# Kernel optimization log

Measured on AMD Instinct MI355X. Metric: run time of the kernel, lower is better.

## Reference

```python
import jax, jax.numpy as jnp
import numpy as np

EPS = 1e-8

def dice(x, alpha):
    # Dice activation (dim=3): per-channel BN (batch stats over B,L axes), then gating.
    m = jnp.mean(x, axis=(0, 1), keepdims=True)
    v = jnp.var(x, axis=(0, 1), keepdims=True)
    p = jax.nn.sigmoid((x - m) * jax.lax.rsqrt(v + EPS))
    return p * x + (1.0 - p) * alpha * x


def setup_inputs() -> dict:
    key = jax.random.key(0)
    ks = jax.random.split(key, 12)
    B, L, D = 2048, 200, 128
    H1, H2 = 128, 32
    query = jax.random.normal(ks[0], (B, D), dtype=jnp.float32)
    keys = jax.random.normal(ks[1], (B, L, D), dtype=jnp.float32)
    keys_len = jax.random.randint(ks[2], (B,), 0, L)
    s1 = 1.0 / np.sqrt(4 * D)
    s2 = 1.0 / np.sqrt(H1)
    s3 = 1.0 / np.sqrt(H2)
    W1 = jax.random.uniform(ks[3], (4 * D, H1), minval=-s1, maxval=s1, dtype=jnp.float32)
    b1 = jax.random.uniform(ks[4], (H1,), minval=-s1, maxval=s1, dtype=jnp.float32)
    alpha1 = jnp.zeros((H1,), dtype=jnp.float32)
    W2 = jax.random.uniform(ks[5], (H1, H2), minval=-s2, maxval=s2, dtype=jnp.float32)
    b2 = jax.random.uniform(ks[6], (H2,), minval=-s2, maxval=s2, dtype=jnp.float32)
    alpha2 = jnp.zeros((H2,), dtype=jnp.float32)
    Wd = jax.random.uniform(ks[7], (H2, 1), minval=-s3, maxval=s3, dtype=jnp.float32)
    bd = jax.random.uniform(ks[8], (1,), minval=-s3, maxval=s3, dtype=jnp.float32)
    return {"query": query, "keys": keys, "keys_len": keys_len,
            "W1": W1, "b1": b1, "alpha1": alpha1,
            "W2": W2, "b2": b2, "alpha2": alpha2,
            "Wd": Wd, "bd": bd}


def reference(query, keys, keys_len, W1, b1, alpha1, W2, b2, alpha2, Wd, bd):
    B, L, D = keys.shape
    q = jnp.broadcast_to(query[:, None, :], (B, L, D))
    # concat/diff/product features -> (B, L, 4D)
    x = jnp.concatenate([q, keys, q - keys, q * keys], axis=-1)
    h = dice(x @ W1 + b1, alpha1)
    h = dice(h @ W2 + b2, alpha2)
    score = (h @ Wd + bd)[..., 0]            # (B, L)
    mask = jnp.arange(L) < keys_len[:, None]  # (B, L)
    score = jnp.where(mask, score, 0.0)
    # weighted-sum pooling: (B, L) x (B, L, D) -> (B, D)
    return jnp.einsum('bl,bld->bd', score, keys)
```

## Files before the change

### kernel.cpp

```cpp
#include <hip/hip_runtime.h>
#include <hip/hip_bf16.h>
#include <stdint.h>

typedef __attribute__((ext_vector_type(8))) short bf16x8;
typedef __attribute__((ext_vector_type(4))) float f32x4;

#define B_SZ 2048
#define L_SZ 200
#define D_SZ 128
#define NROWS (B_SZ * L_SZ)
#define NTILES (NROWS / 16)

__device__ __forceinline__ short f2bf(float f) {
    __bf16 h = (__bf16)f;
    return __builtin_bit_cast(short, h);
}
__device__ __forceinline__ float bf2f(short s) {
    union { uint32_t u; float f; } v; v.u = ((uint32_t)(uint16_t)s) << 16;
    return v.f;
}
__device__ __forceinline__ float sigm(float x) {
    return 1.0f / (1.0f + __expf(-x));
}

__global__ void k0_prep(const float* __restrict__ W1, const float* __restrict__ W2,
                        float* __restrict__ Aprime, float* __restrict__ Bf32,
                        float* __restrict__ Cf32, ushort* __restrict__ W2f,
                        float* __restrict__ stats)
{
    const int total = 16384 + 16384 + 16384 + 4096 + 512;
    for (int i = blockIdx.x * blockDim.x + threadIdx.x; i < total; i += gridDim.x * blockDim.x) {
        if (i < 16384) {
            int r = i >> 7, c = i & 127;
            Aprime[i] = W1[r * 128 + c] + W1[(256 + r) * 128 + c];
        } else if (i < 32768) {
            int e = i - 16384;
            int j = e & 7, l = (e >> 3) & 63, kt = (e >> 9) & 3, ct = e >> 11;
            int k = kt * 32 + ((l >> 4) << 3) + j;
            int col = (ct << 4) + (l & 15);
            Bf32[e] = W1[(128 + k) * 128 + col] - W1[(256 + k) * 128 + col];
        } else if (i < 49152) {
            int e = i - 32768;
            int j = e & 7, l = (e >> 3) & 63, kt = (e >> 9) & 3, ct = e >> 11;
            int k = kt * 32 + ((l >> 4) << 3) + j;
            int col = (ct << 4) + (l & 15);
            Cf32[e] = W1[(384 + k) * 128 + col];
        } else if (i < 49152 + 4096) {
            int f = i - 49152;
            int j = f & 7, l = (f >> 3) & 63, kt = (f >> 9) & 3, ct = f >> 11;
            int kk = kt * 32 + ((l >> 4) << 3) + j;
            int col = (ct << 4) + (l & 15);
            W2f[f] = (ushort)f2bf(W2[kk * 32 + col]);
        } else {
            stats[i - (49152 + 4096)] = 0.0f;
        }
    }
}

__global__ void k1_qA(const float* __restrict__ q, const float* __restrict__ Aprime,
                      const float* __restrict__ b1, float* __restrict__ qA)
{
    __shared__ float qs[128];
    int b = blockIdx.x, c = threadIdx.x;
    qs[c] = q[b * 128 + c];
    __syncthreads();
    float acc = b1[c];
    #pragma unroll 8
    for (int r = 0; r < 128; ++r) acc += qs[r] * Aprime[r * 128 + c];
    qA[b * 128 + c] = acc;
}

__global__ void __launch_bounds__(64, 2) k2_main(
    const float* __restrict__ query, const float* __restrict__ keys,
    const float* __restrict__ qA, const float* __restrict__ Bf32,
    const float* __restrict__ Cf32, ushort* __restrict__ z1,
    float* __restrict__ stats1)
{
    const int lane = threadIdx.x;
    const int b = blockIdx.x;
    const int r15 = lane & 15, g = lane >> 4;

    f32x4 qv[4][2];
    #pragma unroll
    for (int kt = 0; kt < 4; ++kt) {
        const float* qp = query + (size_t)b * 128 + kt * 32 + g * 8;
        qv[kt][0] = *(const f32x4*)(qp);
        qv[kt][1] = *(const f32x4*)(qp + 4);
    }

    bf16x8 wb[8][4];
    #pragma unroll
    for (int ct = 0; ct < 8; ++ct)
        #pragma unroll
        for (int kt = 0; kt < 4; ++kt) {
            const int fi = ((ct * 4 + kt) * 64 + lane) * 8;
            f32x4 b0 = *(const f32x4*)(Bf32 + fi);
            f32x4 b1v = *(const f32x4*)(Bf32 + fi + 4);
            f32x4 c0 = *(const f32x4*)(Cf32 + fi);
            f32x4 c1 = *(const f32x4*)(Cf32 + fi + 4);
            bf16x8 w;
            #pragma unroll
            for (int j = 0; j < 4; ++j) {
                w[j]     = f2bf(b0[j]  + qv[kt][0][j] * c0[j]);
                w[4 + j] = f2bf(b1v[j] + qv[kt][1][j] * c1[j]);
            }
            wb[ct][kt] = w;
        }

    float qa[8];
    #pragma unroll
    for (int ct = 0; ct < 8; ++ct) qa[ct] = qA[(size_t)b * 128 + ct * 16 + r15];

    float ssum[8] = {0,0,0,0,0,0,0,0}, ssq[8] = {0,0,0,0,0,0,0,0};

    const float* kbase = keys + (size_t)b * L_SZ * 128;
    ushort* zbase = z1 + (size_t)b * L_SZ * 128;

    for (int t = 0; t < 13; ++t) {
        const int row0 = t * 16;
        const int lrowc = min(row0 + r15, L_SZ - 1);
        const float* kp = kbase + (size_t)lrowc * 128 + g * 8;

        bf16x8 afr[4];
        #pragma unroll
        for (int kt = 0; kt < 4; ++kt) {
            f32x4 k0 = *(const f32x4*)(kp + kt * 32);
            f32x4 k1 = *(const f32x4*)(kp + kt * 32 + 4);
            bf16x8 a;
            #pragma unroll
            for (int j = 0; j < 4; ++j) { a[j] = f2bf(k0[j]); a[4 + j] = f2bf(k1[j]); }
            afr[kt] = a;
        }

        f32x4 acc[8];
        #pragma unroll
        for (int ct = 0; ct < 8; ++ct) {
            acc[ct] = (f32x4){0, 0, 0, 0};
            #pragma unroll
            for (int kt = 0; kt < 4; ++kt)
                acc[ct] = __builtin_amdgcn_mfma_f32_16x16x32_bf16(afr[kt], wb[ct][kt], acc[ct], 0, 0, 0);
        }

        const int rbase = row0 + g * 4;
        #pragma unroll
        for (int j = 0; j < 4; ++j) {
            const int row = rbase + j;
            if (row < L_SZ) {
                #pragma unroll
                for (int ct = 0; ct < 8; ++ct) {
                    float v = acc[ct][j] + qa[ct];
                    ssum[ct] += v;
                    ssq[ct] += v * v;
                    zbase[(size_t)row * 128 + ct * 16 + r15] = (ushort)f2bf(v);
                }
            }
        }
    }

    #pragma unroll
    for (int ct = 0; ct < 8; ++ct) {
        float s = ssum[ct], q2 = ssq[ct];
        s += __shfl_xor(s, 16); s += __shfl_xor(s, 32);
        q2 += __shfl_xor(q2, 16); q2 += __shfl_xor(q2, 32);
        if (g == 0) {
            atomicAdd(&stats1[ct * 16 + r15], s);
            atomicAdd(&stats1[128 + ct * 16 + r15], q2);
        }
    }
}

__global__ void k_fin(const float* __restrict__ raw, float* __restrict__ fin, int nch)
{
    int c = threadIdx.x;
    if (c >= nch) return;
    float n = (float)NROWS;
    float m = raw[c] / n;
    float v = raw[nch + c] / n - m * m;
    float r = rsqrtf(v + 1e-8f);
    fin[c] = r;
    fin[nch + c] = -m * r;
}

__global__ void __launch_bounds__(64, 2) k4_z2(
    const ushort* __restrict__ z1, const ushort* __restrict__ W2f,
    const float* __restrict__ fin1, const float* __restrict__ alpha1,
    const float* __restrict__ b2, float* __restrict__ z2, float* __restrict__ stats2)
{
    const int lane = threadIdx.x, r15 = lane & 15, g = lane >> 4;
    bf16x8 bfr[2][4];
    #pragma unroll
    for (int ct = 0; ct < 2; ++ct)
        #pragma unroll
        for (int kt = 0; kt < 4; ++kt)
            bfr[ct][kt] = *(const bf16x8*)(W2f + ((size_t)(ct * 4 + kt) * 64 + lane) * 8);

    float rstd[4][8], bias0[4][8], alp[4][8];
    #pragma unroll
    for (int kt = 0; kt < 4; ++kt)
        #pragma unroll
        for (int j = 0; j < 8; ++j) {
            int c = kt * 32 + g * 8 + j;
            rstd[kt][j] = fin1[c];
            bias0[kt][j] = fin1[128 + c];
            alp[kt][j] = alpha1[c];
        }
    float b2v[2] = { b2[r15], b2[16 + r15] };
    float ssum[2] = {0, 0}, ssq[2] = {0, 0};

    for (int rt = blockIdx.x; rt < NTILES; rt += gridDim.x) {
        int rowA = rt * 16 + r15;
        bf16x8 afr[4];
        #pragma unroll
        for (int kt = 0; kt < 4; ++kt) {
            bf16x8 zv = *(const bf16x8*)(z1 + (size_t)rowA * 128 + kt * 32 + g * 8);
            bf16x8 hv;
            #pragma unroll
            for (int j = 0; j < 8; ++j) {
                float z = bf2f(zv[j]);
                float zh = z * rstd[kt][j] + bias0[kt][j];
                float p = sigm(zh);
                float t = p + (1.0f - p) * alp[kt][j];
                hv[j] = f2bf(z * t);
            }
            afr[kt] = hv;
        }
        f32x4 acc[2];
        #pragma unroll
        for (int ct = 0; ct < 2; ++ct) {
            acc[ct] = (f32x4){0, 0, 0, 0};
            #pragma unroll
            for (int kt = 0; kt < 4; ++kt)
                acc[ct] = __builtin_amdgcn_mfma_f32_16x16x32_bf16(afr[kt], bfr[ct][kt], acc[ct], 0, 0, 0);
        }
        int rowC = rt * 16 + g * 4;
        #pragma unroll
        for (int j = 0; j < 4; ++j) {
            int row = rowC + j;
            #pragma unroll
            for (int ct = 0; ct < 2; ++ct) {
                float v = acc[ct][j] + b2v[ct];
                ssum[ct] += v;
                ssq[ct] += v * v;
                z2[(size_t)row * 32 + ct * 16 + r15] = v;
            }
        }
    }
    #pragma unroll
    for (int ct = 0; ct < 2; ++ct) {
        float s = ssum[ct], q2 = ssq[ct];
        s += __shfl_xor(s, 16); s += __shfl_xor(s, 32);
        q2 += __shfl_xor(q2, 16); q2 += __shfl_xor(q2, 32);
        if (g == 0) {
            int col = ct * 16 + r15;
            atomicAdd(&stats2[col], s);
            atomicAdd(&stats2[32 + col], q2);
        }
    }
}

__global__ void __launch_bounds__(256) k6_score_pool(
    const float* __restrict__ z2, const float* __restrict__ keys,
    const int* __restrict__ keys_len, const float* __restrict__ fin2,
    const float* __restrict__ alpha2, const float* __restrict__ Wd,
    const float* __restrict__ bd, float* __restrict__ out)
{
    __shared__ float pp[129];
    __shared__ float sc[200];
    __shared__ float part[2][128];
    int b = blockIdx.x, t = threadIdx.x;
    if (t < 64) pp[t] = fin2[t];
    else if (t < 96) pp[t] = alpha2[t - 64];
    else if (t < 128) pp[t] = Wd[t - 96];
    else if (t == 128) pp[128] = bd[0];
    __syncthreads();

    int klen = keys_len[b];
    if (t < 200) {
        float s = 0.0f;
        if (t < klen) {
            const float* zp = z2 + ((size_t)b * 200 + t) * 32;
            f32x4 zr[8];
            #pragma unroll
            for (int i = 0; i < 8; ++i) zr[i] = ((const f32x4*)zp)[i];
            s = pp[128];
            #pragma unroll
            for (int c = 0; c < 32; ++c) {
                float z = zr[c >> 2][c & 3];
                float zh = z * pp[c] + pp[32 + c];
                float p = sigm(zh);
                float h = z * (p + (1.0f - p) * pp[64 + c]);
                s += h * pp[96 + c];
            }
        }
        sc[t] = s;
    }
    __syncthreads();

    int c = t & 127, prt = t >> 7;
    int lim = min(100, klen - prt * 100);
    const float* kp = keys + ((size_t)b * 200 + prt * 100) * 128 + c;
    float acc = 0.0f;
    #pragma unroll 4
    for (int l = 0; l < lim; ++l) acc += sc[prt * 100 + l] * kp[(size_t)l * 128];
    part[prt][c] = acc;
    __syncthreads();
    if (t < 128) out[(size_t)b * 128 + t] = part[0][t] + part[1][t];
}

extern "C" void kernel_launch(void* const* d_in, const int* in_sizes, int n_in,
                              void* d_out, int out_size, void* d_ws, size_t ws_size,
                              hipStream_t stream) {
    const float* query    = (const float*)d_in[0];
    const float* keys     = (const float*)d_in[1];
    const int*   keys_len = (const int*)d_in[2];
    const float* W1       = (const float*)d_in[3];
    const float* b1       = (const float*)d_in[4];
    const float* alpha1   = (const float*)d_in[5];
    const float* W2       = (const float*)d_in[6];
    const float* b2       = (const float*)d_in[7];
    const float* alpha2   = (const float*)d_in[8];
    const float* Wd       = (const float*)d_in[9];
    const float* bd       = (const float*)d_in[10];
    float* out = (float*)d_out;

    char* ws = (char*)d_ws;
    ushort* z1     = (ushort*)(ws);
    float*  z2     = (float*)(ws + 104857600);
    float*  qA     = (float*)(ws + 157286400);
    float*  Aprime = (float*)(ws + 158334976);
    float*  Bf32   = (float*)(ws + 158400512);
    float*  Cf32   = (float*)(ws + 158466048);
    ushort* W2f    = (ushort*)(ws + 158531584);
    float*  stats  = (float*)(ws + 158539776);
    float*  fin1   = (float*)(ws + 158541824);
    float*  fin2   = (float*)(ws + 158542848);

    k0_prep<<<128, 256, 0, stream>>>(W1, W2, Aprime, Bf32, Cf32, W2f, stats);
    k1_qA<<<B_SZ, 128, 0, stream>>>(query, Aprime, b1, qA);
    k2_main<<<B_SZ, 64, 0, stream>>>(query, keys, qA, Bf32, Cf32, z1, stats);
    k_fin<<<1, 128, 0, stream>>>(stats, fin1, 128);
    k4_z2<<<4096, 64, 0, stream>>>(z1, W2f, fin1, alpha1, b2, z2, stats + 256);
    k_fin<<<1, 32, 0, stream>>>(stats + 256, fin2, 32);
    k6_score_pool<<<B_SZ, 256, 0, stream>>>(z2, keys, keys_len, fin2, alpha2, Wd, bd, out);
}
```

Measured before the change: 282.5 us.

## Split k2 across column groups, store z2 as bf16, vectorize k4 param loads

```diff
diff --git a/kernel.cpp b/kernel.cpp
--- a/kernel.cpp
+++ b/kernel.cpp
@@ -3,6 +3,7 @@
 #include <stdint.h>
 
 typedef __attribute__((ext_vector_type(8))) short bf16x8;
+typedef __attribute__((ext_vector_type(8))) unsigned short u16x8;
 typedef __attribute__((ext_vector_type(4))) float f32x4;
 
 #define B_SZ 2048
@@ -70,14 +71,16 @@
     qA[b * 128 + c] = acc;
 }
 
-__global__ void __launch_bounds__(64, 2) k2_main(
+__global__ void __launch_bounds__(64, 4) k2_main(
     const float* __restrict__ query, const float* __restrict__ keys,
     const float* __restrict__ qA, const float* __restrict__ Bf32,
     const float* __restrict__ Cf32, ushort* __restrict__ z1,
     float* __restrict__ stats1)
 {
+    const int p = blockIdx.x;
+    const int b = (p & 7) | ((p >> 5) << 3);
+    const int cg = (p >> 3) & 3;
     const int lane = threadIdx.x;
-    const int b = blockIdx.x;
     const int r15 = lane & 15, g = lane >> 4;
 
     f32x4 qv[4][2];
@@ -88,11 +91,12 @@
         qv[kt][1] = *(const f32x4*)(qp + 4);
     }
 
-    bf16x8 wb[8][4];
-    #pragma unroll
-    for (int ct = 0; ct < 8; ++ct)
+    bf16x8 wb[2][4];
+    #pragma unroll
+    for (int ctl = 0; ctl < 2; ++ctl)
         #pragma unroll
         for (int kt = 0; kt < 4; ++kt) {
+            const int ct = cg * 2 + ctl;
             const int fi = ((ct * 4 + kt) * 64 + lane) * 8;
             f32x4 b0 = *(const f32x4*)(Bf32 + fi);
             f32x4 b1v = *(const f32x4*)(Bf32 + fi + 4);
@@ -104,14 +108,15 @@
                 w[j]     = f2bf(b0[j]  + qv[kt][0][j] * c0[j]);
                 w[4 + j] = f2bf(b1v[j] + qv[kt][1][j] * c1[j]);
             }
-            wb[ct][kt] = w;
-        }
-
-    float qa[8];
-    #pragma unroll
-    for (int ct = 0; ct < 8; ++ct) qa[ct] = qA[(size_t)b * 128 + ct * 16 + r15];
-
-    float ssum[8] = {0,0,0,0,0,0,0,0}, ssq[8] = {0,0,0,0,0,0,0,0};
+            wb[ctl][kt] = w;
+        }
+
+    float qa[2];
+    #pragma unroll
+    for (int ctl = 0; ctl < 2; ++ctl)
+        qa[ctl] = qA[(size_t)b * 128 + (cg * 2 + ctl) * 16 + r15];
+
+    float ssum[2] = {0, 0}, ssq[2] = {0, 0};
 
     const float* kbase = keys + (size_t)b * L_SZ * 128;
     ushort* zbase = z1 + (size_t)b * L_SZ * 128;
@@ -132,13 +137,13 @@
             afr[kt] = a;
         }
 
-        f32x4 acc[8];
-        #pragma unroll
-        for (int ct = 0; ct < 8; ++ct) {
-            acc[ct] = (f32x4){0, 0, 0, 0};
+        f32x4 acc[2];
+        #pragma unroll
+        for (int ctl = 0; ctl < 2; ++ctl) {
+            acc[ctl] = (f32x4){0, 0, 0, 0};
             #pragma unroll
             for (int kt = 0; kt < 4; ++kt)
-                acc[ct] = __builtin_amdgcn_mfma_f32_16x16x32_bf16(afr[kt], wb[ct][kt], acc[ct], 0, 0, 0);
+                acc[ctl] = __builtin_amdgcn_mfma_f32_16x16x32_bf16(afr[kt], wb[ctl][kt], acc[ctl], 0, 0, 0);
         }
 
         const int rbase = row0 + g * 4;
@@ -147,24 +152,25 @@
             const int row = rbase + j;
             if (row < L_SZ) {
                 #pragma unroll
-                for (int ct = 0; ct < 8; ++ct) {
-                    float v = acc[ct][j] + qa[ct];
-                    ssum[ct] += v;
-                    ssq[ct] += v * v;
-                    zbase[(size_t)row * 128 + ct * 16 + r15] = (ushort)f2bf(v);
+                for (int ctl = 0; ctl < 2; ++ctl) {
+                    float v = acc[ctl][j] + qa[ctl];
+                    ssum[ctl] += v;
+                    ssq[ctl] += v * v;
+                    zbase[(size_t)row * 128 + (cg * 2 + ctl) * 16 + r15] = (ushort)f2bf(v);
                 }
             }
         }
     }
 
     #pragma unroll
-    for (int ct = 0; ct < 8; ++ct) {
-        float s = ssum[ct], q2 = ssq[ct];
+    for (int ctl = 0; ctl < 2; ++ctl) {
+        float s = ssum[ctl], q2 = ssq[ctl];
         s += __shfl_xor(s, 16); s += __shfl_xor(s, 32);
         q2 += __shfl_xor(q2, 16); q2 += __shfl_xor(q2, 32);
         if (g == 0) {
-            atomicAdd(&stats1[ct * 16 + r15], s);
-            atomicAdd(&stats1[128 + ct * 16 + r15], q2);
+            const int col = (cg * 2 + ctl) * 16 + r15;
+            atomicAdd(&stats1[col], s);
+            atomicAdd(&stats1[128 + col], q2);
         }
     }
 }
@@ -184,7 +190,7 @@
 __global__ void __launch_bounds__(64, 2) k4_z2(
     const ushort* __restrict__ z1, const ushort* __restrict__ W2f,
     const float* __restrict__ fin1, const float* __restrict__ alpha1,
-    const float* __restrict__ b2, float* __restrict__ z2, float* __restrict__ stats2)
+    const float* __restrict__ b2, ushort* __restrict__ z2, float* __restrict__ stats2)
 {
     const int lane = threadIdx.x, r15 = lane & 15, g = lane >> 4;
     bf16x8 bfr[2][4];
@@ -194,16 +200,17 @@
         for (int kt = 0; kt < 4; ++kt)
             bfr[ct][kt] = *(const bf16x8*)(W2f + ((size_t)(ct * 4 + kt) * 64 + lane) * 8);
 
-    float rstd[4][8], bias0[4][8], alp[4][8];
-    #pragma unroll
-    for (int kt = 0; kt < 4; ++kt)
-        #pragma unroll
-        for (int j = 0; j < 8; ++j) {
-            int c = kt * 32 + g * 8 + j;
-            rstd[kt][j] = fin1[c];
-            bias0[kt][j] = fin1[128 + c];
-            alp[kt][j] = alpha1[c];
-        }
+    f32x4 rstd4[4][2], bias4[4][2], alp4[4][2];
+    #pragma unroll
+    for (int kt = 0; kt < 4; ++kt) {
+        const int base = kt * 32 + g * 8;
+        rstd4[kt][0] = *(const f32x4*)(fin1 + base);
+        rstd4[kt][1] = *(const f32x4*)(fin1 + base + 4);
+        bias4[kt][0] = *(const f32x4*)(fin1 + 128 + base);
+        bias4[kt][1] = *(const f32x4*)(fin1 + 128 + base + 4);
+        alp4[kt][0]  = *(const f32x4*)(alpha1 + base);
+        alp4[kt][1]  = *(const f32x4*)(alpha1 + base + 4);
+    }
     float b2v[2] = { b2[r15], b2[16 + r15] };
     float ssum[2] = {0, 0}, ssq[2] = {0, 0};
 
@@ -215,12 +222,13 @@
             bf16x8 zv = *(const bf16x8*)(z1 + (size_t)rowA * 128 + kt * 32 + g * 8);
             bf16x8 hv;
             #pragma unroll
-            for (int j = 0; j < 8; ++j) {
-                float z = bf2f(zv[j]);
-                float zh = z * rstd[kt][j] + bias0[kt][j];
-                float p = sigm(zh);
-                float t = p + (1.0f - p) * alp[kt][j];
-                hv[j] = f2bf(z * t);
+            for (int jj = 0; jj < 8; ++jj) {
+                const int h = jj >> 2, j = jj & 3;
+                float z = bf2f(zv[jj]);
+                float zh = z * rstd4[kt][h][j] + bias4[kt][h][j];
+                float pgate = sigm(zh);
+                float t = pgate + (1.0f - pgate) * alp4[kt][h][j];
+                hv[jj] = f2bf(z * t);
             }
             afr[kt] = hv;
         }
@@ -241,7 +249,7 @@
                 float v = acc[ct][j] + b2v[ct];
                 ssum[ct] += v;
                 ssq[ct] += v * v;
-                z2[(size_t)row * 32 + ct * 16 + r15] = v;
+                z2[(size_t)row * 32 + ct * 16 + r15] = (ushort)f2bf(v);
             }
         }
     }
@@ -259,7 +267,7 @@
 }
 
 __global__ void __launch_bounds__(256) k6_score_pool(
-    const float* __restrict__ z2, const float* __restrict__ keys,
+    const ushort* __restrict__ z2, const float* __restrict__ keys,
     const int* __restrict__ keys_len, const float* __restrict__ fin2,
     const float* __restrict__ alpha2, const float* __restrict__ Wd,
     const float* __restrict__ bd, float* __restrict__ out)
@@ -278,17 +286,17 @@
     if (t < 200) {
         float s = 0.0f;
         if (t < klen) {
-            const float* zp = z2 + ((size_t)b * 200 + t) * 32;
-            f32x4 zr[8];
-            #pragma unroll
-            for (int i = 0; i < 8; ++i) zr[i] = ((const f32x4*)zp)[i];
+            const ushort* zp = z2 + ((size_t)b * 200 + t) * 32;
+            u16x8 zr[4];
+            #pragma unroll
+            for (int i = 0; i < 4; ++i) zr[i] = ((const u16x8*)zp)[i];
             s = pp[128];
             #pragma unroll
             for (int c = 0; c < 32; ++c) {
-                float z = zr[c >> 2][c & 3];
+                float z = bf2f((short)zr[c >> 3][c & 7]);
                 float zh = z * pp[c] + pp[32 + c];
-                float p = sigm(zh);
-                float h = z * (p + (1.0f - p) * pp[64 + c]);
+                float pg = sigm(zh);
+                float h = z * (pg + (1.0f - pg) * pp[64 + c]);
                 s += h * pp[96 + c];
             }
         }
@@ -325,21 +333,21 @@
 
     char* ws = (char*)d_ws;
     ushort* z1     = (ushort*)(ws);
-    float*  z2     = (float*)(ws + 104857600);
-    float*  qA     = (float*)(ws + 157286400);
-    float*  Aprime = (float*)(ws + 158334976);
-    float*  Bf32   = (float*)(ws + 158400512);
-    float*  Cf32   = (float*)(ws + 158466048);
-    ushort* W2f    = (ushort*)(ws + 158531584);
-    float*  stats  = (float*)(ws + 158539776);
-    float*  fin1   = (float*)(ws + 158541824);
-    float*  fin2   = (float*)(ws + 158542848);
+    ushort* z2     = (ushort*)(ws + 104857600);
+    float*  qA     = (float*)(ws + 131072000);
+    float*  Aprime = (float*)(ws + 132120576);
+    float*  Bf32   = (float*)(ws + 132186112);
+    float*  Cf32   = (float*)(ws + 132251648);
+    ushort* W2f    = (ushort*)(ws + 132317184);
+    float*  stats  = (float*)(ws + 132325376);
+    float*  fin1   = (float*)(ws + 132327424);
+    float*  fin2   = (float*)(ws + 132328448);
 
     k0_prep<<<128, 256, 0, stream>>>(W1, W2, Aprime, Bf32, Cf32, W2f, stats);
     k1_qA<<<B_SZ, 128, 0, stream>>>(query, Aprime, b1, qA);
-    k2_main<<<B_SZ, 64, 0, stream>>>(query, keys, qA, Bf32, Cf32, z1, stats);
+    k2_main<<<8192, 64, 0, stream>>>(query, keys, qA, Bf32, Cf32, z1, stats);
     k_fin<<<1, 128, 0, stream>>>(stats, fin1, 128);
-    k4_z2<<<4096, 64, 0, stream>>>(z1, W2f, fin1, alpha1, b2, z2, stats + 256);
+    k4_z2<<<5120, 64, 0, stream>>>(z1, W2f, fin1, alpha1, b2, z2, stats + 256);
     k_fin<<<1, 32, 0, stream>>>(stats + 256, fin2, 32);
     k6_score_pool<<<B_SZ, 256, 0, stream>>>(z2, keys, keys_len, fin2, alpha2, Wd, bd, out);
 }
```

New measurement: 313.1 us. 1.11x slower.
